# Performance work log

Hardware: AMD Instinct MI355X
Metric: run time of the kernel (lower is better)

Reference implementation:

```python
import jax, jax.numpy as jnp
import numpy as np

D = 1024      # in_features
H = 768       # hidden_features per routed expert
E = 8         # n_routed_experts
K = 2         # n_activated_experts
NS = 2        # n_shared_experts
ROUTE_SCALE = 1.0


def setup_inputs() -> dict:
    key = jax.random.key(0)
    ks = jax.random.split(key, 6)
    s = 0.02
    return {
        "x": jax.random.normal(ks[0], (2, 1024, D), jnp.float32),
        "gate_w": jax.random.normal(ks[1], (E, D), jnp.float32) * s,
        "W1": jax.random.normal(ks[2], (E, 2 * H, D), jnp.float32) * s,   # expert fc1 (y|gate)
        "W2": jax.random.normal(ks[3], (E, D, H), jnp.float32) * s,       # expert fc2
        "Ws1": jax.random.normal(ks[4], (2 * NS * H, D), jnp.float32) * s,  # shared fc1
        "Ws2": jax.random.normal(ks[5], (D, NS * H), jnp.float32) * s,      # shared fc2
    }


def _gated_mlp(x, w1, w2):
    # GatedMLP: fc1 -> chunk(2) -> y * silu(gate) -> fc2, all bias-free
    h = x @ w1.T
    y, g = jnp.split(h, 2, axis=-1)
    return (y * jax.nn.silu(g)) @ w2.T


def reference(x, gate_w, W1, W2, Ws1, Ws2):
    x_shape = x.shape
    xf = x.reshape(-1, D)                 # [T, D]
    T = xf.shape[0]

    # --- Gate: softmax scores in fp32, top-k routing ---
    scores = jax.nn.softmax((xf @ gate_w.T).astype(jnp.float32), axis=-1)  # [T, E]
    top_vals, top_idx = jax.lax.top_k(scores, K)
    # no bias branch (in_features != 7168): gathered original scores == top_k values
    weights = (top_vals * ROUTE_SCALE).astype(x.dtype)                      # [T, K]

    # Dense per-token/expert combine weights (0 for unselected experts);
    # mathematically identical to the per-expert gather/scatter-add combine.
    w_dense = jnp.zeros((T, E), x.dtype).at[jnp.arange(T)[:, None], top_idx].set(weights)

    # --- Routed experts (stacked GatedMLPs) ---
    h = jnp.einsum('td,ehd->teh', xf, W1)        # [T, E, 2H]
    y, g = jnp.split(h, 2, axis=-1)
    eo = jnp.einsum('teh,edh->ted', y * jax.nn.silu(g), W2)  # [T, E, D]
    z = jnp.einsum('te,ted->td', w_dense, eo)    # weighted combine

    # --- Shared experts ---
    z = z + _gated_mlp(xf, Ws1, Ws2)
    return z.reshape(x_shape)
```

## Files before the change

kernel.cpp:

```cpp
#include <hip/hip_runtime.h>
#include <hip/hip_bf16.h>


typedef short bf16x8 __attribute__((ext_vector_type(8)));
typedef float f32x4 __attribute__((ext_vector_type(4)));

__device__ __forceinline__ unsigned short f2b(float f) {
    __hip_bfloat16 h = __float2bfloat16(f);
    return *reinterpret_cast<unsigned short*>(&h);
}

__device__ __forceinline__ void ldst16(const unsigned short* g, unsigned short* l) {
    __builtin_amdgcn_global_load_lds(
        (const __attribute__((address_space(1))) unsigned int*)g,
        (__attribute__((address_space(3))) unsigned int*)l, 16, 0, 0);
}

__device__ __forceinline__ void cvt8(const float* s, unsigned short* d, int j) {
    const float4* sp = reinterpret_cast<const float4*>(s) + (size_t)j * 2;
    float4 v0 = sp[0], v1 = sp[1];
    union { unsigned short u[8]; uint4 v; } o;
    o.u[0]=f2b(v0.x); o.u[1]=f2b(v0.y); o.u[2]=f2b(v0.z); o.u[3]=f2b(v0.w);
    o.u[4]=f2b(v1.x); o.u[5]=f2b(v1.y); o.u[6]=f2b(v1.z); o.u[7]=f2b(v1.w);
    *(reinterpret_cast<uint4*>(d) + j) = o.v;
}

__global__ __launch_bounds__(256) void k_convgate(const float* __restrict__ x,
                                                  const float* __restrict__ gw,
                                                  const float* __restrict__ W1,
                                                  const float* __restrict__ Ws1,
                                                  const float* __restrict__ W2,
                                                  const float* __restrict__ Ws2,
                                                  unsigned short* __restrict__ xb,
                                                  unsigned short* __restrict__ W1b,
                                                  unsigned short* __restrict__ Ws1b,
                                                  unsigned short* __restrict__ W2b,
                                                  unsigned short* __restrict__ Ws2b,
                                                  int* __restrict__ tokslot,
                                                  float* __restrict__ wroute,
                                                  int* __restrict__ cnt,
                                                  float* __restrict__ out) {
    __shared__ float red[4][8];
    __shared__ float sc[8];
    const int b = blockIdx.x, tid = threadIdx.x;
    if (b < 11520) {
        int i = b * 256 + tid;
        if (i < 1572864)       cvt8(W1,  W1b,  i);
        else if (i < 1966080)  cvt8(Ws1, Ws1b, i - 1572864);
        else if (i < 2752512)  cvt8(W2,  W2b,  i - 1966080);
        else if (i < 2949120)  cvt8(Ws2, Ws2b, i - 2752512);
        return;
    }
    const int t = b - 11520;
    const int lane = tid & 63, w = tid >> 6;

    float4 v = reinterpret_cast<const float4*>(x + (size_t)t * 1024)[tid];
    union { unsigned short u[4]; } o;
    o.u[0]=f2b(v.x); o.u[1]=f2b(v.y); o.u[2]=f2b(v.z); o.u[3]=f2b(v.w);
    reinterpret_cast<ushort4*>(xb + (size_t)t * 1024)[tid] = *(ushort4*)o.u;

    float p[8];
    for (int e = 0; e < 8; e++) {
        float4 g = reinterpret_cast<const float4*>(gw + (size_t)e * 1024)[tid];
        p[e] = v.x*g.x + v.y*g.y + v.z*g.z + v.w*g.w;
    }
    for (int e = 0; e < 8; e++)
        for (int off = 32; off > 0; off >>= 1) p[e] += __shfl_down(p[e], off, 64);
    if (lane == 0)
        for (int e = 0; e < 8; e++) red[w][e] = p[e];
    __syncthreads();
    if (tid < 8) sc[tid] = red[0][tid] + red[1][tid] + red[2][tid] + red[3][tid];
    __syncthreads();
    if (tid == 0) {
        float m = sc[0];
        for (int e = 1; e < 8; e++) m = fmaxf(m, sc[e]);
        float ex[8], sum = 0.f;
        for (int e = 0; e < 8; e++) { ex[e] = expf(sc[e] - m); sum += ex[e]; }
        float inv = 1.f / sum;
        int i1 = 0;
        for (int e = 1; e < 8; e++) if (sc[e] > sc[i1]) i1 = e;
        int i2 = -1; float s2 = -1e30f;
        for (int e = 0; e < 8; e++) if (e != i1 && sc[e] > s2) { s2 = sc[e]; i2 = e; }
        int p1 = atomicAdd(&cnt[i1 * 16], 1);
        tokslot[i1 * 2048 + p1] = t; wroute[i1 * 2048 + p1] = ex[i1] * inv;
        int p2 = atomicAdd(&cnt[i2 * 16], 1);
        tokslot[i2 * 2048 + p2] = t; wroute[i2 * 2048 + p2] = ex[i2] * inv;
    }
    reinterpret_cast<float4*>(out + (size_t)t * 1024)[tid] = (float4){0.f, 0.f, 0.f, 0.f};
}

__global__ __launch_bounds__(256) void k_fc1u(const unsigned short* __restrict__ xb,
                                              const unsigned short* __restrict__ W1b,
                                              const unsigned short* __restrict__ Ws1b,
                                              const int* __restrict__ tokslot,
                                              const float* __restrict__ wroute,
                                              const int* __restrict__ cnt,
                                              unsigned short* __restrict__ act_r,
                                              unsigned short* __restrict__ acts) {
    __shared__ alignas(16) unsigned short As[128 * 64];
    __shared__ alignas(16) unsigned short Bs[128 * 64];
    const int tid = threadIdx.x, lane = tid & 63, w = tid >> 6;
    const int wr = w >> 1, wc = w & 1;
    const int mt = blockIdx.x / 12, ht = blockIdx.x % 12;

    int pre = 0, sel = -1, base = 0;
    for (int ee = 0; ee < 10; ee++) {
        int til = (ee < 8) ? ((cnt[ee * 16] + 127) >> 7) : 16;
        if (sel < 0 && mt < pre + til) { sel = ee; base = pre; }
        pre += til;
    }
    if (sel < 0) return;
    const int e = sel, m0 = (mt - base) * 128, h0 = ht * 64;
    const int Te = (e < 8) ? cnt[e * 16] : 2048;
    const unsigned short* Bp = (e < 8) ? (W1b + (size_t)e * 1536 * 1024)
                                       : (Ws1b + (size_t)(e - 8) * 768 * 1024);
    const int gOff = (e < 8) ? 768 : 1536;

    const int kc = tid & 7;
    int aoff[4], boff[4];
    for (int q = 0; q < 4; q++) {
        int row = q * 32 + (tid >> 3);
        int idx = m0 + row;
        int tk = (e < 8) ? ((idx < Te) ? tokslot[e * 2048 + idx] : 0) : idx;
        aoff[q] = tk * 1024 + ((kc ^ (row & 7)) << 3);
        int grow = (row < 64) ? (h0 + row) : (gOff + h0 + row - 64);
        boff[q] = grow * 1024 + ((kc ^ (row & 7)) << 3);
    }

    f32x4 accy[4][2], accg[4][2];
    for (int i = 0; i < 4; i++)
        for (int j = 0; j < 2; j++) {
            accy[i][j] = (f32x4){0.f, 0.f, 0.f, 0.f};
            accg[i][j] = (f32x4){0.f, 0.f, 0.f, 0.f};
        }

    for (int k0 = 0; k0 < 1024; k0 += 64) {
        for (int q = 0; q < 4; q++) {
            ldst16(xb + aoff[q] + k0, As + (q * 256 + tid) * 8);
            ldst16(Bp + boff[q] + k0, Bs + (q * 256 + tid) * 8);
        }
        __syncthreads();
        for (int kh = 0; kh < 2; kh++) {
            const int cq = kh * 4 + (lane >> 4);
            bf16x8 a[4], by[2], bg[2];
            for (int i = 0; i < 4; i++) {
                int r = 64 * wr + 16 * i + (lane & 15);
                a[i] = *(const bf16x8*)&As[r * 64 + ((cq ^ (r & 7)) << 3)];
            }
            for (int j = 0; j < 2; j++) {
                int ry = 32 * wc + 16 * j + (lane & 15);
                by[j] = *(const bf16x8*)&Bs[ry * 64 + ((cq ^ (ry & 7)) << 3)];
                int rg = 64 + ry;
                bg[j] = *(const bf16x8*)&Bs[rg * 64 + ((cq ^ (rg & 7)) << 3)];
            }
            for (int i = 0; i < 4; i++)
                for (int j = 0; j < 2; j++) {
                    accy[i][j] = __builtin_amdgcn_mfma_f32_16x16x32_bf16(a[i], by[j], accy[i][j], 0, 0, 0);
                    accg[i][j] = __builtin_amdgcn_mfma_f32_16x16x32_bf16(a[i], bg[j], accg[i][j], 0, 0, 0);
                }
        }
        __syncthreads();
    }

    for (int i = 0; i < 4; i++)
        for (int r = 0; r < 4; r++) {
            int irow = m0 + 64 * wr + 16 * i + ((lane >> 4) << 2) + r;
            if (irow >= Te) continue;
            float sw = (e < 8) ? wroute[e * 2048 + irow] : 1.0f;
            unsigned short* dst = (e < 8)
                ? (act_r + ((size_t)e * 2048 + irow) * 768)
                : (acts + (size_t)irow * 1536 + (size_t)(e - 8) * 768);
            for (int j = 0; j < 2; j++) {
                float y = accy[i][j][r], g = accg[i][j][r];
                float sg = g / (1.0f + __expf(-g));
                int col = h0 + 32 * wc + 16 * j + (lane & 15);
                dst[col] = f2b(sw * y * sg);
            }
        }
}

__global__ __launch_bounds__(256) void k_fc2u(const unsigned short* __restrict__ act_r,
                                              const unsigned short* __restrict__ acts,
                                              const unsigned short* __restrict__ W2b,
                                              const unsigned short* __restrict__ Ws2b,
                                              const int* __restrict__ tokslot,
                                              const int* __restrict__ cnt,
                                              float* __restrict__ out) {
    __shared__ alignas(16) unsigned short As[128 * 128];
    __shared__ alignas(16) unsigned short Bs[64 * 128];
    const int tid = threadIdx.x, lane = tid & 63, w = tid >> 6;
    const int wr = w >> 1, wc = w & 1;
    const int mt = blockIdx.x >> 4, nt = blockIdx.x & 15;

    int pre = 0, sel = -1, base = 0;
    for (int ee = 0; ee < 9; ee++) {
        int til = (ee < 8) ? ((cnt[ee * 16] + 127) >> 7) : 16;
        if (sel < 0 && mt < pre + til) { sel = ee; base = pre; }
        pre += til;
    }
    if (sel < 0) return;
    const int e = sel, m0 = (mt - base) * 128, n0 = nt * 64;
    int Te, astride, bstride, K;
    const unsigned short *Ab, *Bb;
    if (e < 8) {
        Te = cnt[e * 16]; K = 768; astride = 768; bstride = 768;
        Ab = act_r + (size_t)e * 2048 * 768;
        Bb = W2b + (size_t)e * 1024 * 768;
    } else {
        Te = 2048; K = 1536; astride = 1536; bstride = 1536;
        Ab = acts;
        Bb = Ws2b;
    }

    const int cp = tid & 15;
    int aoff[8], boff[4];
    for (int q = 0; q < 8; q++) {
        int row = q * 16 + (tid >> 4);
        aoff[q] = (m0 + row) * astride + ((cp ^ (row & 15)) << 3);
    }
    for (int q = 0; q < 4; q++) {
        int row = q * 16 + (tid >> 4);
        boff[q] = (n0 + row) * bstride + ((cp ^ (row & 15)) << 3);
    }

    f32x4 acc[4][2];
    for (int i = 0; i < 4; i++)
        for (int j = 0; j < 2; j++) acc[i][j] = (f32x4){0.f, 0.f, 0.f, 0.f};

    for (int k0 = 0; k0 < K; k0 += 128) {
        for (int q = 0; q < 8; q++) ldst16(Ab + aoff[q] + k0, As + (q * 256 + tid) * 8);
        for (int q = 0; q < 4; q++) ldst16(Bb + boff[q] + k0, Bs + (q * 256 + tid) * 8);
        __syncthreads();
        for (int kh = 0; kh < 4; kh++) {
            const int cq = kh * 4 + (lane >> 4);
            bf16x8 a[4], b[2];
            for (int i = 0; i < 4; i++) {
                int r = 64 * wr + 16 * i + (lane & 15);
                a[i] = *(const bf16x8*)&As[r * 128 + ((cq ^ (r & 15)) << 3)];
            }
            for (int j = 0; j < 2; j++) {
                int rb = 32 * wc + 16 * j + (lane & 15);
                b[j] = *(const bf16x8*)&Bs[rb * 128 + ((cq ^ (rb & 15)) << 3)];
            }
            for (int i = 0; i < 4; i++)
                for (int j = 0; j < 2; j++)
                    acc[i][j] = __builtin_amdgcn_mfma_f32_16x16x32_bf16(a[i], b[j], acc[i][j], 0, 0, 0);
        }
        __syncthreads();
    }

    for (int i = 0; i < 4; i++)
        for (int r = 0; r < 4; r++) {
            int irow = m0 + 64 * wr + 16 * i + ((lane >> 4) << 2) + r;
            if (irow >= Te) continue;
            int t = (e < 8) ? tokslot[e * 2048 + irow] : irow;
            for (int j = 0; j < 2; j++) {
                int col = n0 + 32 * wc + 16 * j + (lane & 15);
                atomicAdd(out + (size_t)t * 1024 + col, acc[i][j][r]);
            }
        }
}

extern "C" void kernel_launch(void* const* d_in, const int* in_sizes, int n_in,
                              void* d_out, int out_size, void* d_ws, size_t ws_size,
                              hipStream_t stream) {
    const float* x   = (const float*)d_in[0];
    const float* gw  = (const float*)d_in[1];
    const float* W1  = (const float*)d_in[2];
    const float* W2  = (const float*)d_in[3];
    const float* Ws1 = (const float*)d_in[4];
    const float* Ws2 = (const float*)d_in[5];
    float* out = (float*)d_out;

    char* ws = (char*)d_ws;
    unsigned short* xb    = (unsigned short*)(ws + 0);
    unsigned short* W1b   = (unsigned short*)(ws + 4194304);
    unsigned short* Ws1b  = (unsigned short*)(ws + 29360128);
    unsigned short* W2b   = (unsigned short*)(ws + 35651584);
    unsigned short* Ws2b  = (unsigned short*)(ws + 48234496);
    unsigned short* act_r = (unsigned short*)(ws + 51380224);
    unsigned short* acts  = (unsigned short*)(ws + 76546048);
    int*            tokslot = (int*)(ws + 82837504);
    float*          wroute  = (float*)(ws + 82903040);
    int*            cnt     = (int*)(ws + 82968576);

    hipMemsetAsync(cnt, 0, 512, stream);
    k_convgate<<<13568, 256, 0, stream>>>(x, gw, W1, Ws1, W2, Ws2,
                                          xb, W1b, Ws1b, W2b, Ws2b,
                                          tokslot, wroute, cnt, out);
    k_fc1u<<<864, 256, 0, stream>>>(xb, W1b, Ws1b, tokslot, wroute, cnt, act_r, acts);
    k_fc2u<<<896, 256, 0, stream>>>(act_r, acts, W2b, Ws2b, tokslot, cnt, out);
}
```

Measured before the change: 236.3 us.

## Fuse fp32-to-bf16 weight conversion into GEMM tile loads

```diff
diff --git a/kernel.cpp b/kernel.cpp
--- a/kernel.cpp
+++ b/kernel.cpp
@@ -16,48 +16,29 @@
         (__attribute__((address_space(3))) unsigned int*)l, 16, 0, 0);
 }
 
-__device__ __forceinline__ void cvt8(const float* s, unsigned short* d, int j) {
-    const float4* sp = reinterpret_cast<const float4*>(s) + (size_t)j * 2;
-    float4 v0 = sp[0], v1 = sp[1];
+__device__ __forceinline__ uint4 pack8(float4 a, float4 b) {
     union { unsigned short u[8]; uint4 v; } o;
-    o.u[0]=f2b(v0.x); o.u[1]=f2b(v0.y); o.u[2]=f2b(v0.z); o.u[3]=f2b(v0.w);
-    o.u[4]=f2b(v1.x); o.u[5]=f2b(v1.y); o.u[6]=f2b(v1.z); o.u[7]=f2b(v1.w);
-    *(reinterpret_cast<uint4*>(d) + j) = o.v;
-}
-
-__global__ __launch_bounds__(256) void k_convgate(const float* __restrict__ x,
-                                                  const float* __restrict__ gw,
-                                                  const float* __restrict__ W1,
-                                                  const float* __restrict__ Ws1,
-                                                  const float* __restrict__ W2,
-                                                  const float* __restrict__ Ws2,
-                                                  unsigned short* __restrict__ xb,
-                                                  unsigned short* __restrict__ W1b,
-                                                  unsigned short* __restrict__ Ws1b,
-                                                  unsigned short* __restrict__ W2b,
-                                                  unsigned short* __restrict__ Ws2b,
-                                                  int* __restrict__ tokslot,
-                                                  float* __restrict__ wroute,
-                                                  int* __restrict__ cnt,
-                                                  float* __restrict__ out) {
+    o.u[0]=f2b(a.x); o.u[1]=f2b(a.y); o.u[2]=f2b(a.z); o.u[3]=f2b(a.w);
+    o.u[4]=f2b(b.x); o.u[5]=f2b(b.y); o.u[6]=f2b(b.z); o.u[7]=f2b(b.w);
+    return o.v;
+}
+
+__global__ __launch_bounds__(256) void k_gate(const float* __restrict__ x,
+                                              const float* __restrict__ gw,
+                                              unsigned short* __restrict__ xb,
+                                              int* __restrict__ tokslot,
+                                              float* __restrict__ wroute,
+                                              int* __restrict__ cnt,
+                                              float* __restrict__ out) {
     __shared__ float red[4][8];
     __shared__ float sc[8];
-    const int b = blockIdx.x, tid = threadIdx.x;
-    if (b < 11520) {
-        int i = b * 256 + tid;
-        if (i < 1572864)       cvt8(W1,  W1b,  i);
-        else if (i < 1966080)  cvt8(Ws1, Ws1b, i - 1572864);
-        else if (i < 2752512)  cvt8(W2,  W2b,  i - 1966080);
-        else if (i < 2949120)  cvt8(Ws2, Ws2b, i - 2752512);
-        return;
-    }
-    const int t = b - 11520;
+    const int t = blockIdx.x, tid = threadIdx.x;
     const int lane = tid & 63, w = tid >> 6;
 
     float4 v = reinterpret_cast<const float4*>(x + (size_t)t * 1024)[tid];
-    union { unsigned short u[4]; } o;
+    union { unsigned short u[4]; ushort4 v4; } o;
     o.u[0]=f2b(v.x); o.u[1]=f2b(v.y); o.u[2]=f2b(v.z); o.u[3]=f2b(v.w);
-    reinterpret_cast<ushort4*>(xb + (size_t)t * 1024)[tid] = *(ushort4*)o.u;
+    reinterpret_cast<ushort4*>(xb + (size_t)t * 1024)[tid] = o.v4;
 
     float p[8];
     for (int e = 0; e < 8; e++) {
@@ -90,8 +71,8 @@
 }
 
 __global__ __launch_bounds__(256) void k_fc1u(const unsigned short* __restrict__ xb,
-                                              const unsigned short* __restrict__ W1b,
-                                              const unsigned short* __restrict__ Ws1b,
+                                              const float* __restrict__ W1f,
+                                              const float* __restrict__ Ws1f,
                                               const int* __restrict__ tokslot,
                                               const float* __restrict__ wroute,
                                               const int* __restrict__ cnt,
@@ -112,8 +93,8 @@
     if (sel < 0) return;
     const int e = sel, m0 = (mt - base) * 128, h0 = ht * 64;
     const int Te = (e < 8) ? cnt[e * 16] : 2048;
-    const unsigned short* Bp = (e < 8) ? (W1b + (size_t)e * 1536 * 1024)
-                                       : (Ws1b + (size_t)(e - 8) * 768 * 1024);
+    const float* Bpf = (e < 8) ? (W1f + (size_t)e * 1536 * 1024)
+                               : (Ws1f + (size_t)(e - 8) * 768 * 1024);
     const int gOff = (e < 8) ? 768 : 1536;
 
     const int kc = tid & 7;
@@ -135,9 +116,13 @@
         }
 
     for (int k0 = 0; k0 < 1024; k0 += 64) {
+        for (int q = 0; q < 4; q++)
+            ldst16(xb + aoff[q] + k0, As + (q * 256 + tid) * 8);
+        #pragma unroll
         for (int q = 0; q < 4; q++) {
-            ldst16(xb + aoff[q] + k0, As + (q * 256 + tid) * 8);
-            ldst16(Bp + boff[q] + k0, Bs + (q * 256 + tid) * 8);
+            float4 b0 = *reinterpret_cast<const float4*>(Bpf + boff[q] + k0);
+            float4 b1 = *reinterpret_cast<const float4*>(Bpf + boff[q] + k0 + 4);
+            *reinterpret_cast<uint4*>(&Bs[(q * 256 + tid) * 8]) = pack8(b0, b1);
         }
         __syncthreads();
         for (int kh = 0; kh < 2; kh++) {
@@ -181,8 +166,8 @@
 
 __global__ __launch_bounds__(256) void k_fc2u(const unsigned short* __restrict__ act_r,
                                               const unsigned short* __restrict__ acts,
-                                              const unsigned short* __restrict__ W2b,
-                                              const unsigned short* __restrict__ Ws2b,
+                                              const float* __restrict__ W2f,
+                                              const float* __restrict__ Ws2f,
                                               const int* __restrict__ tokslot,
                                               const int* __restrict__ cnt,
                                               float* __restrict__ out) {
@@ -201,15 +186,16 @@
     if (sel < 0) return;
     const int e = sel, m0 = (mt - base) * 128, n0 = nt * 64;
     int Te, astride, bstride, K;
-    const unsigned short *Ab, *Bb;
+    const unsigned short *Ab;
+    const float *Bbf;
     if (e < 8) {
         Te = cnt[e * 16]; K = 768; astride = 768; bstride = 768;
         Ab = act_r + (size_t)e * 2048 * 768;
-        Bb = W2b + (size_t)e * 1024 * 768;
+        Bbf = W2f + (size_t)e * 1024 * 768;
     } else {
         Te = 2048; K = 1536; astride = 1536; bstride = 1536;
         Ab = acts;
-        Bb = Ws2b;
+        Bbf = Ws2f;
     }
 
     const int cp = tid & 15;
@@ -228,8 +214,14 @@
         for (int j = 0; j < 2; j++) acc[i][j] = (f32x4){0.f, 0.f, 0.f, 0.f};
 
     for (int k0 = 0; k0 < K; k0 += 128) {
-        for (int q = 0; q < 8; q++) ldst16(Ab + aoff[q] + k0, As + (q * 256 + tid) * 8);
-        for (int q = 0; q < 4; q++) ldst16(Bb + boff[q] + k0, Bs + (q * 256 + tid) * 8);
+        for (int q = 0; q < 8; q++)
+            ldst16(Ab + aoff[q] + k0, As + (q * 256 + tid) * 8);
+        #pragma unroll
+        for (int q = 0; q < 4; q++) {
+            float4 b0 = *reinterpret_cast<const float4*>(Bbf + boff[q] + k0);
+            float4 b1 = *reinterpret_cast<const float4*>(Bbf + boff[q] + k0 + 4);
+            *reinterpret_cast<uint4*>(&Bs[(q * 256 + tid) * 8]) = pack8(b0, b1);
+        }
         __syncthreads();
         for (int kh = 0; kh < 4; kh++) {
             const int cq = kh * 4 + (lane >> 4);
@@ -274,20 +266,14 @@
 
     char* ws = (char*)d_ws;
     unsigned short* xb    = (unsigned short*)(ws + 0);
-    unsigned short* W1b   = (unsigned short*)(ws + 4194304);
-    unsigned short* Ws1b  = (unsigned short*)(ws + 29360128);
-    unsigned short* W2b   = (unsigned short*)(ws + 35651584);
-    unsigned short* Ws2b  = (unsigned short*)(ws + 48234496);
-    unsigned short* act_r = (unsigned short*)(ws + 51380224);
-    unsigned short* acts  = (unsigned short*)(ws + 76546048);
-    int*            tokslot = (int*)(ws + 82837504);
-    float*          wroute  = (float*)(ws + 82903040);
-    int*            cnt     = (int*)(ws + 82968576);
+    unsigned short* act_r = (unsigned short*)(ws + 4194304);
+    unsigned short* acts  = (unsigned short*)(ws + 29360128);
+    int*            tokslot = (int*)(ws + 35651584);
+    float*          wroute  = (float*)(ws + 35717120);
+    int*            cnt     = (int*)(ws + 35782656);
 
     hipMemsetAsync(cnt, 0, 512, stream);
-    k_convgate<<<13568, 256, 0, stream>>>(x, gw, W1, Ws1, W2, Ws2,
-                                          xb, W1b, Ws1b, W2b, Ws2b,
-                                          tokslot, wroute, cnt, out);
-    k_fc1u<<<864, 256, 0, stream>>>(xb, W1b, Ws1b, tokslot, wroute, cnt, act_r, acts);
-    k_fc2u<<<896, 256, 0, stream>>>(act_r, acts, W2b, Ws2b, tokslot, cnt, out);
-}
+    k_gate<<<2048, 256, 0, stream>>>(x, gw, xb, tokslot, wroute, cnt, out);
+    k_fc1u<<<864, 256, 0, stream>>>(xb, W1, Ws1, tokslot, wroute, cnt, act_r, acts);
+    k_fc2u<<<896, 256, 0, stream>>>(act_r, acts, W2, Ws2, tokslot, cnt, out);
+}
```

Measured after the change: 238.4 us. About the same (+0.9%).

## Overlap fc2 weight conversion with fc1 GEMM and raise MFMA priority

Applied to the files above, without the earlier changes.

```diff
diff --git a/kernel.cpp b/kernel.cpp
--- a/kernel.cpp
+++ b/kernel.cpp
@@ -29,13 +29,9 @@
                                                   const float* __restrict__ gw,
                                                   const float* __restrict__ W1,
                                                   const float* __restrict__ Ws1,
-                                                  const float* __restrict__ W2,
-                                                  const float* __restrict__ Ws2,
                                                   unsigned short* __restrict__ xb,
                                                   unsigned short* __restrict__ W1b,
                                                   unsigned short* __restrict__ Ws1b,
-                                                  unsigned short* __restrict__ W2b,
-                                                  unsigned short* __restrict__ Ws2b,
                                                   int* __restrict__ tokslot,
                                                   float* __restrict__ wroute,
                                                   int* __restrict__ cnt,
@@ -43,21 +39,19 @@
     __shared__ float red[4][8];
     __shared__ float sc[8];
     const int b = blockIdx.x, tid = threadIdx.x;
-    if (b < 11520) {
+    if (b < 7680) {
         int i = b * 256 + tid;
-        if (i < 1572864)       cvt8(W1,  W1b,  i);
-        else if (i < 1966080)  cvt8(Ws1, Ws1b, i - 1572864);
-        else if (i < 2752512)  cvt8(W2,  W2b,  i - 1966080);
-        else if (i < 2949120)  cvt8(Ws2, Ws2b, i - 2752512);
+        if (i < 1572864)  cvt8(W1,  W1b,  i);
+        else              cvt8(Ws1, Ws1b, i - 1572864);
         return;
     }
-    const int t = b - 11520;
+    const int t = b - 7680;
     const int lane = tid & 63, w = tid >> 6;
 
     float4 v = reinterpret_cast<const float4*>(x + (size_t)t * 1024)[tid];
-    union { unsigned short u[4]; } o;
+    union { unsigned short u[4]; ushort4 v4; } o;
     o.u[0]=f2b(v.x); o.u[1]=f2b(v.y); o.u[2]=f2b(v.z); o.u[3]=f2b(v.w);
-    reinterpret_cast<ushort4*>(xb + (size_t)t * 1024)[tid] = *(ushort4*)o.u;
+    reinterpret_cast<ushort4*>(xb + (size_t)t * 1024)[tid] = o.v4;
 
     float p[8];
     for (int e = 0; e < 8; e++) {
@@ -89,9 +83,13 @@
     reinterpret_cast<float4*>(out + (size_t)t * 1024)[tid] = (float4){0.f, 0.f, 0.f, 0.f};
 }
 
-__global__ __launch_bounds__(256) void k_fc1u(const unsigned short* __restrict__ xb,
+__global__ __launch_bounds__(256) void k_fc1w(const unsigned short* __restrict__ xb,
                                               const unsigned short* __restrict__ W1b,
                                               const unsigned short* __restrict__ Ws1b,
+                                              const float* __restrict__ W2,
+                                              const float* __restrict__ Ws2,
+                                              unsigned short* __restrict__ W2b,
+                                              unsigned short* __restrict__ Ws2b,
                                               const int* __restrict__ tokslot,
                                               const float* __restrict__ wroute,
                                               const int* __restrict__ cnt,
@@ -99,7 +97,14 @@
                                               unsigned short* __restrict__ acts) {
     __shared__ alignas(16) unsigned short As[128 * 64];
     __shared__ alignas(16) unsigned short Bs[128 * 64];
-    const int tid = threadIdx.x, lane = tid & 63, w = tid >> 6;
+    const int tid = threadIdx.x;
+    if (blockIdx.x >= 864) {
+        int i = (blockIdx.x - 864) * 256 + tid;
+        if (i < 786432)  cvt8(W2,  W2b,  i);
+        else             cvt8(Ws2, Ws2b, i - 786432);
+        return;
+    }
+    const int lane = tid & 63, w = tid >> 6;
     const int wr = w >> 1, wc = w & 1;
     const int mt = blockIdx.x / 12, ht = blockIdx.x % 12;
 
@@ -153,11 +158,13 @@
                 int rg = 64 + ry;
                 bg[j] = *(const bf16x8*)&Bs[rg * 64 + ((cq ^ (rg & 7)) << 3)];
             }
+            __builtin_amdgcn_s_setprio(1);
             for (int i = 0; i < 4; i++)
                 for (int j = 0; j < 2; j++) {
                     accy[i][j] = __builtin_amdgcn_mfma_f32_16x16x32_bf16(a[i], by[j], accy[i][j], 0, 0, 0);
                     accg[i][j] = __builtin_amdgcn_mfma_f32_16x16x32_bf16(a[i], bg[j], accg[i][j], 0, 0, 0);
                 }
+            __builtin_amdgcn_s_setprio(0);
         }
         __syncthreads();
     }
@@ -242,9 +249,11 @@
                 int rb = 32 * wc + 16 * j + (lane & 15);
                 b[j] = *(const bf16x8*)&Bs[rb * 128 + ((cq ^ (rb & 15)) << 3)];
             }
+            __builtin_amdgcn_s_setprio(1);
             for (int i = 0; i < 4; i++)
                 for (int j = 0; j < 2; j++)
                     acc[i][j] = __builtin_amdgcn_mfma_f32_16x16x32_bf16(a[i], b[j], acc[i][j], 0, 0, 0);
+            __builtin_amdgcn_s_setprio(0);
         }
         __syncthreads();
     }
@@ -285,9 +294,10 @@
     int*            cnt     = (int*)(ws + 82968576);
 
     hipMemsetAsync(cnt, 0, 512, stream);
-    k_convgate<<<13568, 256, 0, stream>>>(x, gw, W1, Ws1, W2, Ws2,
-                                          xb, W1b, Ws1b, W2b, Ws2b,
-                                          tokslot, wroute, cnt, out);
-    k_fc1u<<<864, 256, 0, stream>>>(xb, W1b, Ws1b, tokslot, wroute, cnt, act_r, acts);
+    k_convgate<<<9728, 256, 0, stream>>>(x, gw, W1, Ws1,
+                                         xb, W1b, Ws1b,
+                                         tokslot, wroute, cnt, out);
+    k_fc1w<<<4704, 256, 0, stream>>>(xb, W1b, Ws1b, W2, Ws2, W2b, Ws2b,
+                                     tokslot, wroute, cnt, act_r, acts);
     k_fc2u<<<896, 256, 0, stream>>>(act_r, acts, W2b, Ws2b, tokslot, cnt, out);
 }
```

New measurement: 233.9 us. About the same (-1.0%).
